# Kernel optimization log

Hardware: AMD Instinct MI355X
Metric: run time of the kernel (lower is better)

The kernel has to match this reference:

```python
import jax, jax.numpy as jnp
import numpy as np

N_NODES = 100000
EMB_DIM = 128
N_PAIRS = 1000000
HIDDEN = 256  # spatial_input_dim = 2 * EMB_DIM


def setup_inputs() -> dict:
    key = jax.random.key(0)
    k1, k2, k3, k4 = jax.random.split(key, 4)
    embs = jax.random.normal(k1, (N_NODES, EMB_DIM), dtype=jnp.float32)
    node_indices = jax.random.randint(k2, (N_PAIRS, 2), 0, N_NODES, dtype=jnp.int64)
    # Glorot-ish small init for the classifier weights
    W1 = jax.random.normal(k3, (2 * EMB_DIM, HIDDEN), dtype=jnp.float32) * (1.0 / np.sqrt(2 * EMB_DIM))
    b1 = jnp.zeros((HIDDEN,), dtype=jnp.float32)
    W2 = jax.random.normal(k4, (HIDDEN, 2), dtype=jnp.float32) * (1.0 / np.sqrt(HIDDEN))
    b2 = jnp.zeros((2,), dtype=jnp.float32)
    return {"spatial_nodes_embs": embs, "node_indices": node_indices,
            "W1": W1, "b1": b1, "W2": W2, "b2": b2}


def reference(spatial_nodes_embs, node_indices, W1, b1, W2, b2):
    # Double gather: embs[node_indices] -> [E, 2, D], flatten -> [E, 2*D]
    x = spatial_nodes_embs[node_indices]                 # [E, 2, D]
    x = x.reshape(x.shape[0], -1)                        # [E, 2*D]
    h = jax.nn.relu(x @ W1 + b1)                         # [E, HIDDEN]
    logits = h @ W2 + b2                                 # [E, 2]
    return logits
```

## Files before the change

kernel.cpp:

```cpp
#include <hip/hip_runtime.h>
#include <hip/hip_bf16.h>
#include <cstdint>
#include <cstddef>

typedef unsigned short u16;
typedef __bf16 bf16x8 __attribute__((ext_vector_type(8)));
typedef u16 ushort8 __attribute__((ext_vector_type(8)));
typedef float f32x4 __attribute__((ext_vector_type(4)));

#define EMB_DIM 128
#define KDIM 256
#define HID 256
#define MTILE 64
#define NBLK 512

#define XB       (2 * MTILE * 512)
#define PART_OFF XB
#define B1_OFF   (XB + 2048)
#define AF2_OFF  (XB + 3072)
#define LDS_BYTES (XB + 2048 + 1024 + 8192)

static __device__ __forceinline__ u16 f2bf(float f) {
    uint32_t u = __builtin_bit_cast(uint32_t, f);
    u += 0x7fffu + ((u >> 16) & 1u);
    return (u16)(u >> 16);
}

__global__ void prep_w1(const float* __restrict__ W1, u16* __restrict__ w1p) {
    int id = blockIdx.x * blockDim.x + threadIdx.x;
    int j   = id & 7;
    int l   = (id >> 3) & 63;
    int kki = (id >> 9) & 7;
    int ntg = id >> 12;
    int k = kki * 32 + ((l >> 4) * 8) + j;
    int n = ntg * 16 + (l & 15);
    w1p[id] = f2bf(W1[k * HID + n]);
}

__global__ void prep_w2(const float* __restrict__ W2, u16* __restrict__ w2ap) {
    int id = blockIdx.x * blockDim.x + threadIdx.x;
    if (id >= 4096) return;
    int j   = id & 7;
    int l   = (id >> 3) & 63;
    int kki = id >> 9;
    int m = l & 15;
    int g = (l >> 4) & 3;
    int k = kki * 32 + g * 4 + ((j >> 2) << 4) + (j & 3);
    w2ap[id] = (m < 2) ? f2bf(W2[k * 2 + m]) : (u16)0;
}

__global__ void prep_embs(const float* __restrict__ in, u16* __restrict__ out, int n) {
    int id = blockIdx.x * blockDim.x + threadIdx.x;
    size_t base = (size_t)id * 8;
    if (base + 8 <= (size_t)n) {
        float4 f0 = *reinterpret_cast<const float4*>(in + base);
        float4 f1 = *reinterpret_cast<const float4*>(in + base + 4);
        ushort8 h;
        h[0] = f2bf(f0.x); h[1] = f2bf(f0.y); h[2] = f2bf(f0.z); h[3] = f2bf(f0.w);
        h[4] = f2bf(f1.x); h[5] = f2bf(f1.y); h[6] = f2bf(f1.z); h[7] = f2bf(f1.w);
        *reinterpret_cast<ushort8*>(out + base) = h;
    }
}

static __device__ __forceinline__ void gload_lds16(const void* g, void* s) {
    __builtin_amdgcn_global_load_lds(
        (const __attribute__((address_space(1))) unsigned int*)g,
        (__attribute__((address_space(3))) unsigned int*)s, 16, 0, 0);
}

static __device__ __forceinline__ void stage_tile(const u16* __restrict__ embT,
                                                  int vidx, unsigned char* xb,
                                                  int w, int l) {
    const int row_off = l >> 5;
    const int csel    = (l >> 4) & 1;
    const int c       = l & 31;
    #pragma unroll
    for (int i = 0; i < 8; ++i) {
        int n00 = __builtin_amdgcn_readlane(vidx, 4 * i + 0);
        int n01 = __builtin_amdgcn_readlane(vidx, 4 * i + 1);
        int n10 = __builtin_amdgcn_readlane(vidx, 4 * i + 2);
        int n11 = __builtin_amdgcn_readlane(vidx, 4 * i + 3);
        int na   = csel ? n01 : n00;
        int nb   = csel ? n11 : n10;
        int node = row_off ? nb : na;
        int r2   = 2 * i + row_off;
        int glow = (c ^ (r2 & 7)) & 15;
        const u16* src = embT + (size_t)node * 128 + glow * 8;
        gload_lds16(src, xb + (size_t)(w * 16 + 2 * i) * 512);
    }
}

__launch_bounds__(256, 2)
__global__ void edge_mlp_bf5(const u16* __restrict__ embT,
                             const int* __restrict__ nidx,
                             const u16* __restrict__ w1p,
                             const u16* __restrict__ w2ap,
                             const float* __restrict__ b1,
                             const float* __restrict__ b2,
                             float* __restrict__ out,
                             int npairs, int ntiles, int nb) {
    __shared__ __align__(16) unsigned char lds[LDS_BYTES];
    const int t  = threadIdx.x;
    const int w  = t >> 6;
    const int l  = t & 63;
    const int lg = l >> 4;
    const int lc = l & 15;
    const int gmax = 2 * npairs - 1;

    bf16x8 wf1[4][8];
    #pragma unroll
    for (int ht = 0; ht < 4; ++ht)
        #pragma unroll
        for (int kki = 0; kki < 8; ++kki)
            wf1[ht][kki] = *reinterpret_cast<const bf16x8*>(
                w1p + (size_t)(((w * 4 + ht) * 8 + kki) * 64 + l) * 8);
    #pragma unroll
    for (int ht = 0; ht < 4; ++ht)
        #pragma unroll
        for (int kki = 0; kki < 8; ++kki)
            asm volatile("" : "+v"(wf1[ht][kki]));

    float b2c = b2[t & 1];
    asm volatile("" : "+v"(b2c));

    if (w == 0) {
        gload_lds16(b1 + l * 4, lds + B1_OFF);
    } else if (w == 1) {
        #pragma unroll
        for (int i = 0; i < 8; ++i)
            gload_lds16(w2ap + (size_t)i * 512 + l * 8, lds + AF2_OFF + i * 1024);
    }

    const int base0 = lc * 512 + ((lg ^ (lc & 3)) << 4) + (((lc >> 2) & 1) << 6);

    float2* part = reinterpret_cast<float2*>(lds + PART_OFF);

    int tile = blockIdx.x;

    {
        int gi = 2 * (tile * 64 + w * 16) + l;
        int v0 = nidx[gi < gmax ? gi : gmax];
        stage_tile(embT, v0, lds, w, l);
    }
    int vnext;
    {
        int gi = 2 * ((tile + nb) * 64 + w * 16) + l;
        vnext = nidx[gi < gmax ? gi : gmax];
    }

    int buf = 0;
    for (; tile < ntiles; tile += nb) {
        __syncthreads();

        const int nxt = tile + nb;
        if (nxt < ntiles)
            stage_tile(embT, vnext, lds + (buf ^ 1) * (MTILE * 512), w, l);
        int vfut;
        {
            int gi = 2 * ((nxt + nb) * 64 + w * 16) + l;
            vfut = nidx[gi < gmax ? gi : gmax];
        }

        const int vbuf = base0 + buf * (MTILE * 512);
        f32x4 acc2[4][4] = {};
        #pragma unroll
        for (int kki = 0; kki < 8; ++kki) {
            const int va = vbuf ^ (kki << 6);
            bf16x8 xf[4];
            #pragma unroll
            for (int et = 0; et < 4; ++et)
                xf[et] = *reinterpret_cast<const bf16x8*>(lds + va + et * 8192);
            #pragma unroll
            for (int ht = 0; ht < 4; ++ht)
                #pragma unroll
                for (int et = 0; et < 4; ++et)
                    acc2[ht][et] = __builtin_amdgcn_mfma_f32_16x16x32_bf16(
                        wf1[ht][kki], xf[et], acc2[ht][et], 0, 0, 0);
        }

        float4 b1v[4];
        #pragma unroll
        for (int ht = 0; ht < 4; ++ht)
            b1v[ht] = *reinterpret_cast<const float4*>(
                lds + B1_OFF + (w * 64 + ht * 16 + lg * 4) * 4);
        bf16x8 af2[2];
        #pragma unroll
        for (int kk = 0; kk < 2; ++kk)
            af2[kk] = *reinterpret_cast<const bf16x8*>(
                lds + AF2_OFF + ((w * 2 + kk) * 64 + l) * 16);

        #pragma unroll
        for (int et = 0; et < 4; ++et) {
            uint32_t wd[4][2];
            #pragma unroll
            for (int ht = 0; ht < 4; ++ht) {
                float v0 = fmaxf(acc2[ht][et][0] + b1v[ht].x, 0.0f);
                float v1 = fmaxf(acc2[ht][et][1] + b1v[ht].y, 0.0f);
                float v2 = fmaxf(acc2[ht][et][2] + b1v[ht].z, 0.0f);
                float v3 = fmaxf(acc2[ht][et][3] + b1v[ht].w, 0.0f);
                asm("v_cvt_pk_bf16_f32 %0, %1, %2" : "=v"(wd[ht][0]) : "v"(v0), "v"(v1));
                asm("v_cvt_pk_bf16_f32 %0, %1, %2" : "=v"(wd[ht][1]) : "v"(v2), "v"(v3));
            }
            int4 lo4 = make_int4(wd[0][0], wd[0][1], wd[1][0], wd[1][1]);
            int4 hi4 = make_int4(wd[2][0], wd[2][1], wd[3][0], wd[3][1]);
            f32x4 a3 = {0.0f, 0.0f, 0.0f, 0.0f};
            a3 = __builtin_amdgcn_mfma_f32_16x16x32_bf16(
                af2[0], __builtin_bit_cast(bf16x8, lo4), a3, 0, 0, 0);
            a3 = __builtin_amdgcn_mfma_f32_16x16x32_bf16(
                af2[1], __builtin_bit_cast(bf16x8, hi4), a3, 0, 0, 0);
            if (l < 16)
                part[w * 64 + et * 16 + l] = make_float2(a3[0], a3[1]);
        }

        asm volatile("s_waitcnt lgkmcnt(0)\n\ts_barrier" ::: "memory");

        if (t < 128) {
            const float* pf = reinterpret_cast<const float*>(part);
            float s = b2c + pf[t] + pf[128 + t] + pf[256 + t] + pf[384 + t];
            int m = t >> 1;
            if (tile * 64 + m < npairs)
                out[(size_t)tile * 128 + t] = s;
        }

        vnext = vfut;
        buf ^= 1;
    }
}

__launch_bounds__(256, 2)
__global__ void edge_mlp_f32g(const float* __restrict__ embs,
                              const int* __restrict__ nidx,
                              const u16* __restrict__ w1p,
                              const float* __restrict__ b1,
                              const float* __restrict__ W2,
                              const float* __restrict__ b2,
                              float* __restrict__ out,
                              int npairs) {
    __shared__ __align__(16) unsigned char lds[MTILE * 512 + 4 * MTILE * 2 * 4];
    const int t  = threadIdx.x;
    const int e0 = blockIdx.x * MTILE;
    {
        const int row = t >> 2;
        const int seg = t & 3;
        const int e = e0 + row;
        if (e < npairs) {
            const int i0 = nidx[2 * e];
            const int i1 = nidx[2 * e + 1];
            const float* src = (seg < 2) ? (embs + (size_t)i0 * EMB_DIM)
                                         : (embs + (size_t)i1 * EMB_DIM);
            const int cbase = (seg & 1) * 64;
            #pragma unroll
            for (int j = 0; j < 8; ++j) {
                const int c = cbase + j * 8;
                float4 f0 = *reinterpret_cast<const float4*>(src + c);
                float4 f1 = *reinterpret_cast<const float4*>(src + c + 4);
                ushort8 h;
                h[0] = f2bf(f0.x); h[1] = f2bf(f0.y);
                h[2] = f2bf(f0.z); h[3] = f2bf(f0.w);
                h[4] = f2bf(f1.x); h[5] = f2bf(f1.y);
                h[6] = f2bf(f1.z); h[7] = f2bf(f1.w);
                int off = row * 512 + (seg * 64 + j * 8) * 2;
                off ^= (row & 7) << 4;
                *reinterpret_cast<ushort8*>(lds + off) = h;
            }
        }
    }
    __syncthreads();
    const int w  = t >> 6;
    const int l  = t & 63;
    const int lg = l >> 4;
    const int lc = l & 15;
    f32x4 acc[4][4] = {};
    #pragma unroll
    for (int kki = 0; kki < 8; ++kki) {
        const int krow = kki * 32 + lg * 8;
        bf16x8 a[4], b[4];
        #pragma unroll
        for (int mt = 0; mt < 4; ++mt) {
            const int row = mt * 16 + lc;
            int off = row * 512 + krow * 2;
            off ^= (row & 7) << 4;
            a[mt] = *reinterpret_cast<const bf16x8*>(lds + off);
        }
        #pragma unroll
        for (int nt = 0; nt < 4; ++nt)
            b[nt] = *reinterpret_cast<const bf16x8*>(
                w1p + (size_t)(((w * 4 + nt) * 8 + kki) * 64 + l) * 8);
        #pragma unroll
        for (int mt = 0; mt < 4; ++mt)
            #pragma unroll
            for (int nt = 0; nt < 4; ++nt)
                acc[mt][nt] = __builtin_amdgcn_mfma_f32_16x16x32_bf16(
                    a[mt], b[nt], acc[mt][nt], 0, 0, 0);
    }
    float p0[4][4] = {}, p1[4][4] = {};
    #pragma unroll
    for (int nt = 0; nt < 4; ++nt) {
        const int n = w * 64 + nt * 16 + lc;
        const float bnv  = b1[n];
        const float w20 = W2[2 * n];
        const float w21 = W2[2 * n + 1];
        #pragma unroll
        for (int mt = 0; mt < 4; ++mt)
            #pragma unroll
            for (int r = 0; r < 4; ++r) {
                float v = fmaxf(acc[mt][nt][r] + bnv, 0.0f);
                p0[mt][r] = fmaf(v, w20, p0[mt][r]);
                p1[mt][r] = fmaf(v, w21, p1[mt][r]);
            }
    }
    #pragma unroll
    for (int mt = 0; mt < 4; ++mt)
        #pragma unroll
        for (int r = 0; r < 4; ++r) {
            float a0 = p0[mt][r], a1 = p1[mt][r];
            #pragma unroll
            for (int mask = 1; mask < 16; mask <<= 1) {
                a0 += __shfl_xor(a0, mask);
                a1 += __shfl_xor(a1, mask);
            }
            p0[mt][r] = a0; p1[mt][r] = a1;
        }
    float* part = reinterpret_cast<float*>(lds + MTILE * 512);
    if (lc == 0) {
        #pragma unroll
        for (int mt = 0; mt < 4; ++mt)
            #pragma unroll
            for (int r = 0; r < 4; ++r) {
                const int m = mt * 16 + lg * 4 + r;
                part[(w * MTILE + m) * 2 + 0] = p0[mt][r];
                part[(w * MTILE + m) * 2 + 1] = p1[mt][r];
            }
    }
    __syncthreads();
    if (t < 2 * MTILE) {
        const int m = t >> 1, c = t & 1;
        if (e0 + m < npairs) {
            float s = b2[c];
            #pragma unroll
            for (int ww = 0; ww < 4; ++ww)
                s += part[(ww * MTILE + m) * 2 + c];
            out[(size_t)(e0 + m) * 2 + c] = s;
        }
    }
}

extern "C" void kernel_launch(void* const* d_in, const int* in_sizes, int n_in,
                              void* d_out, int out_size, void* d_ws, size_t ws_size,
                              hipStream_t stream) {
    const float* embs = (const float*)d_in[0];
    const int*   nidx = (const int*)d_in[1];
    const float* W1   = (const float*)d_in[2];
    const float* b1   = (const float*)d_in[3];
    const float* W2   = (const float*)d_in[4];
    const float* b2   = (const float*)d_in[5];
    float* out = (float*)d_out;

    u16* w1p = (u16*)d_ws;
    prep_w1<<<(KDIM * HID) / 256, 256, 0, stream>>>(W1, w1p);

    const int npairs = in_sizes[1] / 2;
    const int ntiles = (npairs + MTILE - 1) / MTILE;

    const size_t w2_off   = 131072;
    const size_t embT_off = 131072 + 8192;
    const size_t need = embT_off + (size_t)in_sizes[0] * sizeof(u16);
    if (ws_size >= need) {
        u16* w2ap = (u16*)((char*)d_ws + w2_off);
        u16* embT = (u16*)((char*)d_ws + embT_off);
        prep_w2<<<16, 256, 0, stream>>>(W2, w2ap);
        const int nemb = in_sizes[0];
        prep_embs<<<(nemb + 2047) / 2048, 256, 0, stream>>>(embs, embT, nemb);
        const int nb = NBLK < ntiles ? NBLK : ntiles;
        edge_mlp_bf5<<<nb, 256, 0, stream>>>(embT, nidx, w1p, w2ap, b1, b2,
                                             out, npairs, ntiles, nb);
    } else {
        edge_mlp_f32g<<<ntiles, 256, 0, stream>>>(embs, nidx, w1p, b1, W2, b2,
                                                  out, npairs);
    }
}
```

Before: 153.1 us.

## Bucket-sort edge pairs by first node before fused gather-MLP kernel

Adds a counting sort (histogram, scan, scatter) that groups edge pairs by the high bits of their first node index, then runs a new MLP kernel over the sorted pairs. Each block processes a contiguous range of tiles and writes results back through the saved original edge ids. The goal is better cache locality for the embedding gathers. In exchange it adds four extra kernel launches, atomics, extra index traffic and scattered output writes. Sorting only on the first node leaves the second gather random.

Result: slower. 408.9 us (+167.1%).

```diff
diff --git a/kernel.cpp b/kernel.cpp
--- a/kernel.cpp
+++ b/kernel.cpp
@@ -13,6 +13,7 @@
 #define HID 256
 #define MTILE 64
 #define NBLK 512
+#define NBUCK 1024
 
 #define XB       (2 * MTILE * 512)
 #define PART_OFF XB
@@ -59,6 +60,58 @@
         h[0] = f2bf(f0.x); h[1] = f2bf(f0.y); h[2] = f2bf(f0.z); h[3] = f2bf(f0.w);
         h[4] = f2bf(f1.x); h[5] = f2bf(f1.y); h[6] = f2bf(f1.z); h[7] = f2bf(f1.w);
         *reinterpret_cast<ushort8*>(out + base) = h;
+    }
+}
+
+__global__ void k_zero(int* __restrict__ histcur,
+                       int* __restrict__ spairs, int* __restrict__ seid,
+                       int npairs, int ntiles) {
+    int t = threadIdx.x;
+    for (int i = t; i < 2 * NBUCK; i += 256) histcur[i] = 0;
+    for (int i = npairs * 2 + t; i < ntiles * 128; i += 256) spairs[i] = 0;
+    for (int i = npairs + t; i < ntiles * 64; i += 256) seid[i] = 0;
+}
+
+__global__ void k_hist(const int* __restrict__ nidx, int npairs, int* __restrict__ hist) {
+    __shared__ int lh[NBUCK];
+    int t = threadIdx.x;
+    for (int i = t; i < NBUCK; i += 256) lh[i] = 0;
+    __syncthreads();
+    int stride = gridDim.x * blockDim.x;
+    for (int e = blockIdx.x * blockDim.x + t; e < npairs; e += stride)
+        atomicAdd(&lh[((const int2*)nidx)[e].x >> 7], 1);
+    __syncthreads();
+    for (int i = t; i < NBUCK; i += 256)
+        if (lh[i]) atomicAdd(&hist[i], lh[i]);
+}
+
+__global__ void k_scan(const int* __restrict__ hist, int* __restrict__ cursor) {
+    __shared__ int lsum[256];
+    int t = threadIdx.x;
+    int4 h = ((const int4*)hist)[t];
+    int s3 = h.x + h.y + h.z + h.w;
+    lsum[t] = s3;
+    __syncthreads();
+    for (int off = 1; off < 256; off <<= 1) {
+        int v = (t >= off) ? lsum[t - off] : 0;
+        __syncthreads();
+        lsum[t] += v;
+        __syncthreads();
+    }
+    int base = (t > 0) ? lsum[t - 1] : 0;
+    ((int4*)cursor)[t] = make_int4(base, base + h.x, base + h.x + h.y,
+                                   base + h.x + h.y + h.z);
+}
+
+__global__ void k_scatter(const int* __restrict__ nidx, int npairs,
+                          int* __restrict__ cursor,
+                          int2* __restrict__ spairs, int* __restrict__ seid) {
+    int stride = gridDim.x * blockDim.x;
+    for (int e = blockIdx.x * blockDim.x + threadIdx.x; e < npairs; e += stride) {
+        int2 p = ((const int2*)nidx)[e];
+        int pos = atomicAdd(&cursor[p.x >> 7], 1);
+        spairs[pos] = p;
+        seid[pos] = e;
     }
 }
 
@@ -91,21 +144,29 @@
 }
 
 __launch_bounds__(256, 2)
-__global__ void edge_mlp_bf5(const u16* __restrict__ embT,
-                             const int* __restrict__ nidx,
+__global__ void edge_mlp_bf6(const u16* __restrict__ embT,
+                             const int* __restrict__ spairs,
+                             const int* __restrict__ seid,
                              const u16* __restrict__ w1p,
                              const u16* __restrict__ w2ap,
                              const float* __restrict__ b1,
                              const float* __restrict__ b2,
                              float* __restrict__ out,
-                             int npairs, int ntiles, int nb) {
+                             int npairs, int ntiles, int q, int r) {
     __shared__ __align__(16) unsigned char lds[LDS_BYTES];
     const int t  = threadIdx.x;
     const int w  = t >> 6;
     const int l  = t & 63;
     const int lg = l >> 4;
     const int lc = l & 15;
-    const int gmax = 2 * npairs - 1;
+    const int amax = ntiles * 128 - 1;
+    const int smax = ntiles * 64 - 1;
+
+    const int b = blockIdx.x;
+    const int t0  = b * q + (b < r ? b : r);
+    const int len = q + (b < r ? 1 : 0);
+    if (len == 0) return;
+    const int t1 = t0 + len;
 
     bf16x8 wf1[4][8];
     #pragma unroll
@@ -132,33 +193,33 @@
     }
 
     const int base0 = lc * 512 + ((lg ^ (lc & 3)) << 4) + (((lc >> 2) & 1) << 6);
-
     float2* part = reinterpret_cast<float2*>(lds + PART_OFF);
 
-    int tile = blockIdx.x;
-
     {
-        int gi = 2 * (tile * 64 + w * 16) + l;
-        int v0 = nidx[gi < gmax ? gi : gmax];
+        int gi = 2 * (t0 * 64 + w * 16) + l;
+        int v0 = spairs[gi < amax ? gi : amax];
         stage_tile(embT, v0, lds, w, l);
     }
-    int vnext;
+    int vnext, eidcur;
     {
-        int gi = 2 * ((tile + nb) * 64 + w * 16) + l;
-        vnext = nidx[gi < gmax ? gi : gmax];
+        int gi = 2 * ((t0 + 1) * 64 + w * 16) + l;
+        vnext = spairs[gi < amax ? gi : amax];
+        int si = t0 * 64 + ((t & 127) >> 1);
+        eidcur = seid[si < smax ? si : smax];
     }
 
     int buf = 0;
-    for (; tile < ntiles; tile += nb) {
+    for (int tile = t0; tile < t1; ++tile) {
         __syncthreads();
 
-        const int nxt = tile + nb;
-        if (nxt < ntiles)
+        if (tile + 1 < t1)
             stage_tile(embT, vnext, lds + (buf ^ 1) * (MTILE * 512), w, l);
-        int vfut;
+        int vfut, eidnext;
         {
-            int gi = 2 * ((nxt + nb) * 64 + w * 16) + l;
-            vfut = nidx[gi < gmax ? gi : gmax];
+            int gi = 2 * ((tile + 2) * 64 + w * 16) + l;
+            vfut = spairs[gi < amax ? gi : amax];
+            int si = (tile + 1) * 64 + ((t & 127) >> 1);
+            eidnext = seid[si < smax ? si : smax];
         }
 
         const int vbuf = base0 + buf * (MTILE * 512);
@@ -214,6 +275,134 @@
 
         asm volatile("s_waitcnt lgkmcnt(0)\n\ts_barrier" ::: "memory");
 
+        if (t < 128 && tile * 64 + (t >> 1) < npairs) {
+            const float* pf = reinterpret_cast<const float*>(part);
+            float s = b2c + pf[t] + pf[128 + t] + pf[256 + t] + pf[384 + t];
+            out[(size_t)eidcur * 2 + (t & 1)] = s;
+        }
+
+        vnext = vfut;
+        eidcur = eidnext;
+        buf ^= 1;
+    }
+}
+
+__launch_bounds__(256, 2)
+__global__ void edge_mlp_bf5(const u16* __restrict__ embT,
+                             const int* __restrict__ nidx,
+                             const u16* __restrict__ w1p,
+                             const u16* __restrict__ w2ap,
+                             const float* __restrict__ b1,
+                             const float* __restrict__ b2,
+                             float* __restrict__ out,
+                             int npairs, int ntiles, int nb) {
+    __shared__ __align__(16) unsigned char lds[LDS_BYTES];
+    const int t  = threadIdx.x;
+    const int w  = t >> 6;
+    const int l  = t & 63;
+    const int lg = l >> 4;
+    const int lc = l & 15;
+    const int gmax = 2 * npairs - 1;
+
+    bf16x8 wf1[4][8];
+    #pragma unroll
+    for (int ht = 0; ht < 4; ++ht)
+        #pragma unroll
+        for (int kki = 0; kki < 8; ++kki)
+            wf1[ht][kki] = *reinterpret_cast<const bf16x8*>(
+                w1p + (size_t)(((w * 4 + ht) * 8 + kki) * 64 + l) * 8);
+    #pragma unroll
+    for (int ht = 0; ht < 4; ++ht)
+        #pragma unroll
+        for (int kki = 0; kki < 8; ++kki)
+            asm volatile("" : "+v"(wf1[ht][kki]));
+
+    float b2c = b2[t & 1];
+    asm volatile("" : "+v"(b2c));
+
+    if (w == 0) {
+        gload_lds16(b1 + l * 4, lds + B1_OFF);
+    } else if (w == 1) {
+        #pragma unroll
+        for (int i = 0; i < 8; ++i)
+            gload_lds16(w2ap + (size_t)i * 512 + l * 8, lds + AF2_OFF + i * 1024);
+    }
+
+    const int base0 = lc * 512 + ((lg ^ (lc & 3)) << 4) + (((lc >> 2) & 1) << 6);
+    float2* part = reinterpret_cast<float2*>(lds + PART_OFF);
+
+    int tile = blockIdx.x;
+    {
+        int gi = 2 * (tile * 64 + w * 16) + l;
+        int v0 = nidx[gi < gmax ? gi : gmax];
+        stage_tile(embT, v0, lds, w, l);
+    }
+    int vnext;
+    {
+        int gi = 2 * ((tile + nb) * 64 + w * 16) + l;
+        vnext = nidx[gi < gmax ? gi : gmax];
+    }
+
+    int buf = 0;
+    for (; tile < ntiles; tile += nb) {
+        __syncthreads();
+        const int nxt = tile + nb;
+        if (nxt < ntiles)
+            stage_tile(embT, vnext, lds + (buf ^ 1) * (MTILE * 512), w, l);
+        int vfut;
+        {
+            int gi = 2 * ((nxt + nb) * 64 + w * 16) + l;
+            vfut = nidx[gi < gmax ? gi : gmax];
+        }
+        const int vbuf = base0 + buf * (MTILE * 512);
+        f32x4 acc2[4][4] = {};
+        #pragma unroll
+        for (int kki = 0; kki < 8; ++kki) {
+            const int va = vbuf ^ (kki << 6);
+            bf16x8 xf[4];
+            #pragma unroll
+            for (int et = 0; et < 4; ++et)
+                xf[et] = *reinterpret_cast<const bf16x8*>(lds + va + et * 8192);
+            #pragma unroll
+            for (int ht = 0; ht < 4; ++ht)
+                #pragma unroll
+                for (int et = 0; et < 4; ++et)
+                    acc2[ht][et] = __builtin_amdgcn_mfma_f32_16x16x32_bf16(
+                        wf1[ht][kki], xf[et], acc2[ht][et], 0, 0, 0);
+        }
+        float4 b1v[4];
+        #pragma unroll
+        for (int ht = 0; ht < 4; ++ht)
+            b1v[ht] = *reinterpret_cast<const float4*>(
+                lds + B1_OFF + (w * 64 + ht * 16 + lg * 4) * 4);
+        bf16x8 af2[2];
+        #pragma unroll
+        for (int kk = 0; kk < 2; ++kk)
+            af2[kk] = *reinterpret_cast<const bf16x8*>(
+                lds + AF2_OFF + ((w * 2 + kk) * 64 + l) * 16);
+        #pragma unroll
+        for (int et = 0; et < 4; ++et) {
+            uint32_t wd[4][2];
+            #pragma unroll
+            for (int ht = 0; ht < 4; ++ht) {
+                float v0 = fmaxf(acc2[ht][et][0] + b1v[ht].x, 0.0f);
+                float v1 = fmaxf(acc2[ht][et][1] + b1v[ht].y, 0.0f);
+                float v2 = fmaxf(acc2[ht][et][2] + b1v[ht].z, 0.0f);
+                float v3 = fmaxf(acc2[ht][et][3] + b1v[ht].w, 0.0f);
+                asm("v_cvt_pk_bf16_f32 %0, %1, %2" : "=v"(wd[ht][0]) : "v"(v0), "v"(v1));
+                asm("v_cvt_pk_bf16_f32 %0, %1, %2" : "=v"(wd[ht][1]) : "v"(v2), "v"(v3));
+            }
+            int4 lo4 = make_int4(wd[0][0], wd[0][1], wd[1][0], wd[1][1]);
+            int4 hi4 = make_int4(wd[2][0], wd[2][1], wd[3][0], wd[3][1]);
+            f32x4 a3 = {0.0f, 0.0f, 0.0f, 0.0f};
+            a3 = __builtin_amdgcn_mfma_f32_16x16x32_bf16(
+                af2[0], __builtin_bit_cast(bf16x8, lo4), a3, 0, 0, 0);
+            a3 = __builtin_amdgcn_mfma_f32_16x16x32_bf16(
+                af2[1], __builtin_bit_cast(bf16x8, hi4), a3, 0, 0, 0);
+            if (l < 16)
+                part[w * 64 + et * 16 + l] = make_float2(a3[0], a3[1]);
+        }
+        asm volatile("s_waitcnt lgkmcnt(0)\n\ts_barrier" ::: "memory");
         if (t < 128) {
             const float* pf = reinterpret_cast<const float*>(part);
             float s = b2c + pf[t] + pf[128 + t] + pf[256 + t] + pf[384 + t];
@@ -221,7 +410,6 @@
             if (tile * 64 + m < npairs)
                 out[(size_t)tile * 128 + t] = s;
         }
-
         vnext = vfut;
         buf ^= 1;
     }
@@ -274,7 +462,7 @@
     #pragma unroll
     for (int kki = 0; kki < 8; ++kki) {
         const int krow = kki * 32 + lg * 8;
-        bf16x8 a[4], b[4];
+        bf16x8 a[4], bb[4];
         #pragma unroll
         for (int mt = 0; mt < 4; ++mt) {
             const int row = mt * 16 + lc;
@@ -284,52 +472,52 @@
         }
         #pragma unroll
         for (int nt = 0; nt < 4; ++nt)
-            b[nt] = *reinterpret_cast<const bf16x8*>(
+            bb[nt] = *reinterpret_cast<const bf16x8*>(
                 w1p + (size_t)(((w * 4 + nt) * 8 + kki) * 64 + l) * 8);
         #pragma unroll
         for (int mt = 0; mt < 4; ++mt)
             #pragma unroll
             for (int nt = 0; nt < 4; ++nt)
                 acc[mt][nt] = __builtin_amdgcn_mfma_f32_16x16x32_bf16(
-                    a[mt], b[nt], acc[mt][nt], 0, 0, 0);
+                    a[mt], bb[nt], acc[mt][nt], 0, 0, 0);
     }
     float p0[4][4] = {}, p1[4][4] = {};
     #pragma unroll
     for (int nt = 0; nt < 4; ++nt) {
         const int n = w * 64 + nt * 16 + lc;
-        const float bnv  = b1[n];
+        const float bnv = b1[n];
         const float w20 = W2[2 * n];
         const float w21 = W2[2 * n + 1];
         #pragma unroll
         for (int mt = 0; mt < 4; ++mt)
             #pragma unroll
-            for (int r = 0; r < 4; ++r) {
-                float v = fmaxf(acc[mt][nt][r] + bnv, 0.0f);
-                p0[mt][r] = fmaf(v, w20, p0[mt][r]);
-                p1[mt][r] = fmaf(v, w21, p1[mt][r]);
+            for (int rr = 0; rr < 4; ++rr) {
+                float v = fmaxf(acc[mt][nt][rr] + bnv, 0.0f);
+                p0[mt][rr] = fmaf(v, w20, p0[mt][rr]);
+                p1[mt][rr] = fmaf(v, w21, p1[mt][rr]);
             }
     }
     #pragma unroll
     for (int mt = 0; mt < 4; ++mt)
         #pragma unroll
-        for (int r = 0; r < 4; ++r) {
-            float a0 = p0[mt][r], a1 = p1[mt][r];
+        for (int rr = 0; rr < 4; ++rr) {
+            float a0 = p0[mt][rr], a1 = p1[mt][rr];
             #pragma unroll
             for (int mask = 1; mask < 16; mask <<= 1) {
                 a0 += __shfl_xor(a0, mask);
                 a1 += __shfl_xor(a1, mask);
             }
-            p0[mt][r] = a0; p1[mt][r] = a1;
+            p0[mt][rr] = a0; p1[mt][rr] = a1;
         }
     float* part = reinterpret_cast<float*>(lds + MTILE * 512);
     if (lc == 0) {
         #pragma unroll
         for (int mt = 0; mt < 4; ++mt)
             #pragma unroll
-            for (int r = 0; r < 4; ++r) {
-                const int m = mt * 16 + lg * 4 + r;
-                part[(w * MTILE + m) * 2 + 0] = p0[mt][r];
-                part[(w * MTILE + m) * 2 + 1] = p1[mt][r];
+            for (int rr = 0; rr < 4; ++rr) {
+                const int m = mt * 16 + lg * 4 + rr;
+                part[(w * MTILE + m) * 2 + 0] = p0[mt][rr];
+                part[(w * MTILE + m) * 2 + 1] = p1[mt][rr];
             }
     }
     __syncthreads();
@@ -356,24 +544,48 @@
     const float* b2   = (const float*)d_in[5];
     float* out = (float*)d_out;
 
+    const int nemb   = in_sizes[0];
+    const int npairs = in_sizes[1] / 2;
+    const int ntiles = (npairs + MTILE - 1) / MTILE;
+
     u16* w1p = (u16*)d_ws;
     prep_w1<<<(KDIM * HID) / 256, 256, 0, stream>>>(W1, w1p);
 
-    const int npairs = in_sizes[1] / 2;
-    const int ntiles = (npairs + MTILE - 1) / MTILE;
-
     const size_t w2_off   = 131072;
-    const size_t embT_off = 131072 + 8192;
-    const size_t need = embT_off + (size_t)in_sizes[0] * sizeof(u16);
-    if (ws_size >= need) {
+    const size_t hist_off = w2_off + 8192;
+    const size_t cur_off  = hist_off + NBUCK * 4;
+    const size_t embT_off = cur_off + NBUCK * 4;
+    const size_t embT_end = embT_off + (size_t)nemb * 2;
+    const size_t sp_off   = (embT_end + 255) & ~(size_t)255;
+    const size_t se_off   = sp_off + (size_t)ntiles * 128 * 4;
+    const size_t need_sort = se_off + (size_t)ntiles * 64 * 4;
+    const size_t need_bf   = embT_end;
+
+    if (ws_size >= need_bf) {
         u16* w2ap = (u16*)((char*)d_ws + w2_off);
         u16* embT = (u16*)((char*)d_ws + embT_off);
         prep_w2<<<16, 256, 0, stream>>>(W2, w2ap);
-        const int nemb = in_sizes[0];
         prep_embs<<<(nemb + 2047) / 2048, 256, 0, stream>>>(embs, embT, nemb);
-        const int nb = NBLK < ntiles ? NBLK : ntiles;
-        edge_mlp_bf5<<<nb, 256, 0, stream>>>(embT, nidx, w1p, w2ap, b1, b2,
-                                             out, npairs, ntiles, nb);
+
+        if (ws_size >= need_sort) {
+            int* hist    = (int*)((char*)d_ws + hist_off);
+            int* cursor  = (int*)((char*)d_ws + cur_off);
+            int* spairs  = (int*)((char*)d_ws + sp_off);
+            int* seid    = (int*)((char*)d_ws + se_off);
+            k_zero<<<1, 256, 0, stream>>>(hist, spairs, seid, npairs, ntiles);
+            k_hist<<<256, 256, 0, stream>>>(nidx, npairs, hist);
+            k_scan<<<1, 256, 0, stream>>>(hist, cursor);
+            k_scatter<<<256, 256, 0, stream>>>(nidx, npairs, cursor,
+                                               (int2*)spairs, seid);
+            const int nb = NBLK < ntiles ? NBLK : ntiles;
+            const int q = ntiles / nb, rr = ntiles % nb;
+            edge_mlp_bf6<<<nb, 256, 0, stream>>>(embT, spairs, seid, w1p, w2ap,
+                                                 b1, b2, out, npairs, ntiles, q, rr);
+        } else {
+            const int nb = NBLK < ntiles ? NBLK : ntiles;
+            edge_mlp_bf5<<<nb, 256, 0, stream>>>(embT, nidx, w1p, w2ap, b1, b2,
+                                                 out, npairs, ntiles, nb);
+        }
     } else {
         edge_mlp_f32g<<<ntiles, 256, 0, stream>>>(embs, nidx, w1p, b1, W2, b2,
                                                   out, npairs);
```
